# Kernel optimization log

Measured on AMD Instinct MI355X. Metric: run time of the kernel, lower is better.

Reference implementation:

```python
import jax, jax.numpy as jnp
import numpy as np

P_DROP = 0.6  # dropout prob from the source module
N_NODES = 50000
N_EDGES = 800000


def _cheb_edge_weights(edge_index, num_nodes):
    # ChebConv with sym normalization and default lambda_max=2.0:
    # scaled Laplacian hat(L) = 2L/lambda_max - I = -D^{-1/2} A D^{-1/2}
    # (diagonal becomes 0), so edge weight = -1/sqrt(deg[row]*deg[col]).
    row, col = edge_index[0], edge_index[1]
    deg = jnp.zeros((num_nodes,), jnp.float32).at[row].add(1.0)
    dis = jnp.where(deg > 0, jax.lax.rsqrt(jnp.maximum(deg, 1.0)), 0.0)
    return -dis[row] * dis[col]


def _prop(x, row, col, w, n):
    # hat(L) @ x via gather-scale-scatter over the edge list
    return jnp.zeros((n, x.shape[1]), x.dtype).at[row].add(w[:, None] * x[col])


def _cheb_conv(x, row, col, w, W, b, n):
    # Chebyshev recursion: Tx0 = x, Tx1 = hat(L) x, Tx_k = 2 hat(L) Tx_{k-1} - Tx_{k-2}
    Tx0 = x
    out = Tx0 @ W[0]
    Tx1 = _prop(Tx0, row, col, w, n)
    out = out + Tx1 @ W[1]
    for k in range(2, W.shape[0]):
        Tx2 = 2.0 * _prop(Tx1, row, col, w, n) - Tx0
        out = out + Tx2 @ W[k]
        Tx0, Tx1 = Tx1, Tx2
    return out + b


def _dropout(x, key, p):
    keep = jax.random.bernoulli(key, 1.0 - p, x.shape)
    return jnp.where(keep, x * (1.0 / (1.0 - p)), 0.0)


def setup_inputs() -> dict:
    key = jax.random.key(0)
    ks = jax.random.split(key, 8)
    x = jax.random.normal(ks[0], (N_NODES, 64), jnp.float32)
    edge_index = jax.random.randint(ks[1], (2, N_EDGES), 0, N_NODES, jnp.int64)
    W0 = jax.random.normal(ks[2], (2, 64, 64), jnp.float32) * 0.1
    b0 = jnp.zeros((64,), jnp.float32)
    W1 = jax.random.normal(ks[3], (2, 64, 64), jnp.float32) * 0.1
    b1 = jnp.zeros((64,), jnp.float32)
    W2 = jax.random.normal(ks[4], (2, 64, 32), jnp.float32) * 0.1
    b2 = jnp.zeros((32,), jnp.float32)
    return {"x": x, "edge_index": edge_index, "W0": W0, "b0": b0,
            "W1": W1, "b1": b1, "W2": W2, "b2": b2}


def reference(x, edge_index, W0, b0, W1, b1, W2, b2):
    row, col = edge_index[0], edge_index[1]
    n = x.shape[0]
    w = _cheb_edge_weights(edge_index, n)
    dkey = jax.random.key(1)
    params = [(W0, b0), (W1, b1), (W2, b2)]
    for i, (W, b) in enumerate(params):
        x = _dropout(x, jax.random.fold_in(dkey, i), P_DROP)
        x = _cheb_conv(x, row, col, w, W, b, n)
        if i < len(params) - 1:
            x = jax.nn.relu(x)
    return x
```

## Files before the change

kernel.cpp:

```cpp
#include <hip/hip_runtime.h>
#include <stdint.h>

typedef _Float16 half8 __attribute__((ext_vector_type(8)));
typedef float float4v __attribute__((ext_vector_type(4)));

__host__ __device__ inline void tf2x32(uint32_t k0, uint32_t k1,
                                       uint32_t x0, uint32_t x1,
                                       uint32_t* o0, uint32_t* o1) {
  const uint32_t ks2 = k0 ^ k1 ^ 0x1BD11BDAu;
#define ROTL(v, s) (((v) << (s)) | ((v) >> (32 - (s))))
#define RND(r) do { x0 += x1; x1 = ROTL(x1, r); x1 ^= x0; } while (0)
  x0 += k0; x1 += k1;
  RND(13); RND(15); RND(26); RND(6);
  x0 += k1; x1 += ks2 + 1u;
  RND(17); RND(29); RND(16); RND(24);
  x0 += ks2; x1 += k0 + 2u;
  RND(13); RND(15); RND(26); RND(6);
  x0 += k0; x1 += k1 + 3u;
  RND(17); RND(29); RND(16); RND(24);
  x0 += k1; x1 += ks2 + 4u;
  RND(13); RND(15); RND(26); RND(6);
  x0 += ks2; x1 += k0 + 5u;
  *o0 = x0; *o1 = x1;
#undef RND
#undef ROTL
}

__device__ inline bool drop_keep(uint32_t k0, uint32_t k1, uint32_t idx) {
  uint32_t o0, o1;
  tf2x32(k0, k1, 0u, idx, &o0, &o1);
  uint32_t bits = o0 ^ o1;
  float u = __uint_as_float((bits >> 9) | 0x3f800000u) - 1.0f;
  return u < 0.4f;
}

__global__ void k_fill2(const int* __restrict__ row, const int* __restrict__ col,
                        int* __restrict__ cnt, uint16_t* __restrict__ cs, int e,
                        const float* __restrict__ W0, const float* __restrict__ W1,
                        const float* __restrict__ W2, _Float16* __restrict__ wh) {
  int i = blockIdx.x * 256 + threadIdx.x;
  if (blockIdx.x < 80) {
    int d = i;
    if (d < 8192) {
      int o = d >> 7, k = d & 127;
      wh[d] = (_Float16)W0[k * 64 + o];
    } else if (d < 16384) {
      int d1 = d - 8192, o = d1 >> 7, k = d1 & 127;
      wh[d] = (_Float16)W1[k * 64 + o];
    } else if (d < 20480) {
      int d2 = d - 16384, o = d2 >> 7, k = d2 & 127;
      wh[d] = (_Float16)W2[k * 32 + o];
    }
  }
  if (i < e) {
    int r = row[i];
    int pos = atomicAdd(&cnt[r], 1);
    if (pos < 64) cs[(r << 6) + pos] = (uint16_t)col[i];
  }
}

__global__ void k_drop(const float* __restrict__ x, const int* __restrict__ cnt,
                       uint16_t* __restrict__ cs, float* __restrict__ dis,
                       _Float16* __restrict__ y, _Float16* __restrict__ ys,
                       _Float16* __restrict__ ysb, uint32_t k0, uint32_t k1,
                       int n, int nd) {
  int i = blockIdx.x * 256 + threadIdx.x;
  if (i < 64) {
    ys[((size_t)n << 6) + i]  = (_Float16)0.f;
    ysb[((size_t)n << 6) + i] = (_Float16)0.f;
  }
  if (i < nd) {
    const int r = i >> 6;
    const int t = i & 63;
    const int d = cnt[r];
    const float dis_r = (d > 0) ? rsqrtf((float)d) : 0.0f;
    float v = drop_keep(k0, k1, (uint32_t)i) ? x[i] * 2.5f : 0.0f;
    y[i]  = (_Float16)v;
    ys[i] = (_Float16)(dis_r * v);
    if (t == 0) dis[r] = dis_r;
    const int cn = d < 64 ? d : 64;
    const int rnd = (cn + 7) & ~7;
    if (t >= cn && t < rnd) cs[(r << 6) + t] = (uint16_t)n;
  }
}

template<int COUT, bool RELU, bool DROPN, bool WBF>
__global__ __launch_bounds__(256, 8) void k_conv(
    const _Float16* __restrict__ yg, const _Float16* __restrict__ ysg,
    const int* __restrict__ cnt, const uint16_t* __restrict__ cs,
    const float* __restrict__ dis, const _Float16* __restrict__ wt,
    const float* __restrict__ b, float* __restrict__ outf,
    _Float16* __restrict__ outb, _Float16* __restrict__ outs,
    uint32_t nk0, uint32_t nk1, int n) {
  constexpr int R  = 16;
  constexpr int TS = 136;
  __shared__ __align__(16) _Float16 xp[R][TS];

  const int wave = threadIdx.x >> 6;
  const int t    = threadIdx.x & 63;
  const int row0 = blockIdx.x * R;

  for (int i = 0; i < 4; ++i) {
    const int rl = wave * 4 + i;
    const int r  = row0 + rl;
    if (r < n) {
      float acc = 0.0f;
      const int d   = cnt[r];
      const int cn  = d < 64 ? d : 64;
      const int rnd = (cn + 7) & ~7;
      const int base = r << 6;
      for (int j = 0; j < rnd; j += 8) {
        const uint4 cc = *(const uint4*)&cs[base + j];
        uint32_t c[8];
        c[0] = cc.x & 0xffffu; c[1] = cc.x >> 16;
        c[2] = cc.y & 0xffffu; c[3] = cc.y >> 16;
        c[4] = cc.z & 0xffffu; c[5] = cc.z >> 16;
        c[6] = cc.w & 0xffffu; c[7] = cc.w >> 16;
        _Float16 xv[8];
        #pragma unroll
        for (int k = 0; k < 8; ++k) xv[k] = ysg[(c[k] << 6) + t];
        #pragma unroll
        for (int k = 0; k < 8; ++k) acc += (float)xv[k];
      }
      xp[rl][t]      = yg[(uint32_t)(r << 6) + t];
      xp[rl][64 + t] = (_Float16)(-dis[r] * acc);
    }
  }
  __syncthreads();

  constexpr int NW = COUT / 16;
  const int nn   = t & 15;
  const int quad = t >> 4;
  if (wave < NW) {
    const int colg = wave * 16 + nn;
    float4v acc = {0.f, 0.f, 0.f, 0.f};
    #pragma unroll
    for (int ks = 0; ks < 4; ++ks) {
      half8 a  = *(const half8*)&xp[nn][quad * 8 + 32 * ks];
      half8 bb = *(const half8*)&wt[(size_t)colg * 128 + quad * 8 + 32 * ks];
      acc = __builtin_amdgcn_mfma_f32_16x16x32_f16(a, bb, acc, 0, 0, 0);
    }
    const float bias = b[colg];
    #pragma unroll
    for (int rg = 0; rg < 4; ++rg) {
      const int rl = quad * 4 + rg;
      const int rr = row0 + rl;
      if (rr < n) {
        float v = acc[rg] + bias;
        if (RELU) v = fmaxf(v, 0.0f);
        if (DROPN) {
          if (drop_keep(nk0, nk1, (uint32_t)(rr * 64 + colg))) v *= 2.5f;
          else v = 0.0f;
        }
        if (WBF) {
          outb[(size_t)rr * COUT + colg] = (_Float16)v;
          outs[(size_t)rr * COUT + colg] = (_Float16)(dis[rr] * v);
        } else {
          outf[(size_t)rr * COUT + colg] = v;
        }
      }
    }
  }
}

extern "C" void kernel_launch(void* const* d_in, const int* in_sizes, int n_in,
                              void* d_out, int out_size, void* d_ws, size_t ws_size,
                              hipStream_t stream) {
  const float* x   = (const float*)d_in[0];
  const int*   ei  = (const int*)d_in[1];
  const float* W0  = (const float*)d_in[2];
  const float* b0  = (const float*)d_in[3];
  const float* W1f = (const float*)d_in[4];
  const float* b1  = (const float*)d_in[5];
  const float* W2  = (const float*)d_in[6];
  const float* b2  = (const float*)d_in[7];
  float* out = (float*)d_out;

  const int n = in_sizes[0] / 64;
  const int e = in_sizes[1] / 2;
  const int* row = ei;
  const int* col = ei + e;

  size_t off = 0;
  auto carve = [&](size_t elems) {
    size_t o = off;
    off += (elems + 255) & ~(size_t)255;
    return o;
  };
  int* base = (int*)d_ws;
  int*      cnt = base + carve(n);
  float*    dis = (float*)(base + carve(n));
  uint16_t* cs  = (uint16_t*)(base + carve((size_t)n * 32));
  _Float16* ya  = (_Float16*)(base + carve((size_t)n * 32));
  _Float16* ysa = (_Float16*)(base + carve((size_t)(n + 1) * 32));
  _Float16* yb  = (_Float16*)(base + carve((size_t)n * 32));
  _Float16* ysb = (_Float16*)(base + carve((size_t)(n + 1) * 32));
  _Float16* wh  = (_Float16*)(base + carve(10240));
  (void)ws_size;
  _Float16* wh0 = wh;
  _Float16* wh1 = wh + 8192;
  _Float16* wh2 = wh + 16384;

  uint32_t dk[3][2];
  for (uint32_t i = 0; i < 3; ++i) tf2x32(0u, 1u, 0u, i, &dk[i][0], &dk[i][1]);

  hipMemsetAsync(cnt, 0, (size_t)n * 4, stream);

  const int be = (e + 255) / 256;
  const int bd = ((n * 64) + 255) / 256;
  const int bc = (n + 15) / 16;

  k_fill2<<<be, 256, 0, stream>>>(row, col, cnt, cs, e, W0, W1f, W2, wh);
  k_drop<<<bd, 256, 0, stream>>>(x, cnt, cs, dis, ya, ysa, ysb,
                                 dk[0][0], dk[0][1], n, n * 64);

  k_conv<64, true,  true,  true ><<<bc, 256, 0, stream>>>(
      ya, ysa, cnt, cs, dis, wh0, b0, nullptr, yb, ysb, dk[1][0], dk[1][1], n);
  k_conv<64, true,  true,  true ><<<bc, 256, 0, stream>>>(
      yb, ysb, cnt, cs, dis, wh1, b1, nullptr, ya, ysa, dk[2][0], dk[2][1], n);
  k_conv<32, false, false, false><<<bc, 256, 0, stream>>>(
      ya, ysa, cnt, cs, dis, wh2, b2, out, nullptr, nullptr, 0u, 0u, n);
}
```

Before: 232.6 us.

## Partition edge fill by XCD row ownership and unroll neighbor gather by 16

New measurement: 211.2 us. 9.2% less time.

```diff
diff --git a/kernel.cpp b/kernel.cpp
--- a/kernel.cpp
+++ b/kernel.cpp
@@ -35,11 +35,28 @@
 }
 
 __global__ void k_fill2(const int* __restrict__ row, const int* __restrict__ col,
-                        int* __restrict__ cnt, uint16_t* __restrict__ cs, int e,
-                        const float* __restrict__ W0, const float* __restrict__ W1,
-                        const float* __restrict__ W2, _Float16* __restrict__ wh) {
+                        int* __restrict__ cnt, uint16_t* __restrict__ cs,
+                        int e, int rows_per_xcd) {
+  const int owner = blockIdx.x & 7;
+  const int i = (blockIdx.x >> 3) * 256 + threadIdx.x;
+  if (i < e) {
+    int r = row[i];
+    if (r / rows_per_xcd == owner) {
+      int pos = atomicAdd(&cnt[r], 1);
+      if (pos < 64) cs[(r << 6) + pos] = (uint16_t)col[i];
+    }
+  }
+}
+
+__global__ void k_drop(const float* __restrict__ x, const int* __restrict__ cnt,
+                       uint16_t* __restrict__ cs, float* __restrict__ dis,
+                       _Float16* __restrict__ y, _Float16* __restrict__ ys,
+                       _Float16* __restrict__ ysb, uint32_t k0, uint32_t k1,
+                       int n, int nd,
+                       const float* __restrict__ W0, const float* __restrict__ W1,
+                       const float* __restrict__ W2, _Float16* __restrict__ wh) {
   int i = blockIdx.x * 256 + threadIdx.x;
-  if (blockIdx.x < 80) {
+  if (i < 20480) {
     int d = i;
     if (d < 8192) {
       int o = d >> 7, k = d & 127;
@@ -47,24 +64,11 @@
     } else if (d < 16384) {
       int d1 = d - 8192, o = d1 >> 7, k = d1 & 127;
       wh[d] = (_Float16)W1[k * 64 + o];
-    } else if (d < 20480) {
+    } else {
       int d2 = d - 16384, o = d2 >> 7, k = d2 & 127;
       wh[d] = (_Float16)W2[k * 32 + o];
     }
   }
-  if (i < e) {
-    int r = row[i];
-    int pos = atomicAdd(&cnt[r], 1);
-    if (pos < 64) cs[(r << 6) + pos] = (uint16_t)col[i];
-  }
-}
-
-__global__ void k_drop(const float* __restrict__ x, const int* __restrict__ cnt,
-                       uint16_t* __restrict__ cs, float* __restrict__ dis,
-                       _Float16* __restrict__ y, _Float16* __restrict__ ys,
-                       _Float16* __restrict__ ysb, uint32_t k0, uint32_t k1,
-                       int n, int nd) {
-  int i = blockIdx.x * 256 + threadIdx.x;
   if (i < 64) {
     ys[((size_t)n << 6) + i]  = (_Float16)0.f;
     ysb[((size_t)n << 6) + i] = (_Float16)0.f;
@@ -109,7 +113,26 @@
       const int cn  = d < 64 ? d : 64;
       const int rnd = (cn + 7) & ~7;
       const int base = r << 6;
-      for (int j = 0; j < rnd; j += 8) {
+      int j = 0;
+      for (; j + 16 <= rnd; j += 16) {
+        const uint4 c0 = *(const uint4*)&cs[base + j];
+        const uint4 c1 = *(const uint4*)&cs[base + j + 8];
+        uint32_t c[16];
+        c[0]  = c0.x & 0xffffu; c[1]  = c0.x >> 16;
+        c[2]  = c0.y & 0xffffu; c[3]  = c0.y >> 16;
+        c[4]  = c0.z & 0xffffu; c[5]  = c0.z >> 16;
+        c[6]  = c0.w & 0xffffu; c[7]  = c0.w >> 16;
+        c[8]  = c1.x & 0xffffu; c[9]  = c1.x >> 16;
+        c[10] = c1.y & 0xffffu; c[11] = c1.y >> 16;
+        c[12] = c1.z & 0xffffu; c[13] = c1.z >> 16;
+        c[14] = c1.w & 0xffffu; c[15] = c1.w >> 16;
+        _Float16 xv[16];
+        #pragma unroll
+        for (int k = 0; k < 16; ++k) xv[k] = ysg[(c[k] << 6) + t];
+        #pragma unroll
+        for (int k = 0; k < 16; ++k) acc += (float)xv[k];
+      }
+      if (j < rnd) {
         const uint4 cc = *(const uint4*)&cs[base + j];
         uint32_t c[8];
         c[0] = cc.x & 0xffffu; c[1] = cc.x >> 16;
@@ -206,13 +229,15 @@
 
   hipMemsetAsync(cnt, 0, (size_t)n * 4, stream);
 
-  const int be = (e + 255) / 256;
+  const int nchunk = (e + 255) / 256;
   const int bd = ((n * 64) + 255) / 256;
   const int bc = (n + 15) / 16;
-
-  k_fill2<<<be, 256, 0, stream>>>(row, col, cnt, cs, e, W0, W1f, W2, wh);
+  const int rpx = (n + 7) / 8;
+
+  k_fill2<<<nchunk * 8, 256, 0, stream>>>(row, col, cnt, cs, e, rpx);
   k_drop<<<bd, 256, 0, stream>>>(x, cnt, cs, dis, ya, ysa, ysb,
-                                 dk[0][0], dk[0][1], n, n * 64);
+                                 dk[0][0], dk[0][1], n, n * 64,
+                                 W0, W1f, W2, wh);
 
   k_conv<64, true,  true,  true ><<<bc, 256, 0, stream>>>(
       ya, ysa, cnt, cs, dis, wh0, b0, nullptr, yb, ysb, dk[1][0], dk[1][1], n);
```
